# Kernel optimization log

Measured on AMD Instinct MI355X. Metric: run time of the kernel, lower is better.

The kernel has to match this reference:

```python
import jax, jax.numpy as jnp
import numpy as np

B = 2048            # reactions per batch
NODES_PER_MOL = 32
N = B * NODES_PER_MOL   # 65536 nodes per slot graph
E = 2 * N               # 131072 edges per slot graph
NODE_IN, EDGE_IN, H = 64, 16, 300
DEPTH = 3


def setup_inputs() -> dict:
    key = jax.random.key(0)
    ks = jax.random.split(key, 24)
    d = {}
    for i, s in enumerate(["r1", "r2", "p1"]):
        d[f"x_{s}"] = jax.random.normal(ks[4 * i], (N, NODE_IN), jnp.float32)
        d[f"e_{s}"] = jax.random.normal(ks[4 * i + 1], (E, EDGE_IN), jnp.float32)
        d[f"src_{s}"] = jax.random.randint(ks[4 * i + 2], (E,), 0, N, jnp.int32)
        d[f"dst_{s}"] = jax.random.randint(ks[4 * i + 3], (E,), 0, N, jnp.int32)
        d[f"seg_{s}"] = jnp.repeat(jnp.arange(B, dtype=jnp.int32), NODES_PER_MOL)
    s = 0.05
    d["Wn"] = jax.random.normal(ks[12], (NODE_IN, H), jnp.float32) * s
    d["bn"] = jnp.zeros((H,), jnp.float32)
    d["We"] = jax.random.normal(ks[13], (EDGE_IN, H), jnp.float32) * s
    d["be"] = jnp.zeros((H,), jnp.float32)
    d["W1"] = jax.random.normal(ks[14], (DEPTH, H, H), jnp.float32) * s
    d["b1"] = jnp.zeros((DEPTH, H), jnp.float32)
    d["W2"] = jax.random.normal(ks[15], (DEPTH, H, H), jnp.float32) * s
    d["b2"] = jnp.zeros((DEPTH, H), jnp.float32)
    return d


def _gin(x, e, src, dst, Wn, bn, We, be, W1, b1, W2, b2):
    # project_node_feats = Linear + ReLU ; project_edge_feats = Linear
    h = jax.nn.relu(x @ Wn + bn)           # [N, H]
    eh = e @ We + be                        # [E, H]
    n = x.shape[0]
    for l in range(DEPTH):
        # GINEConv (eps=0): agg = sum_{j->i} relu(h_j + e_ji); h = MLP(h + agg)
        m = jax.nn.relu(h[src] + eh)        # [E, H]
        agg = jax.ops.segment_sum(m, dst, num_segments=n)
        z = h + agg
        z = jax.nn.relu(z @ W1[l] + b1[l]) @ W2[l] + b2[l]
        if l < DEPTH - 1:
            z = jax.nn.relu(z)              # inter-layer ReLU (dropout = eval no-op)
        h = z
    return h


def reference(x_r1, e_r1, src_r1, dst_r1, seg_r1,
              x_r2, e_r2, src_r2, dst_r2, seg_r2,
              x_p1, e_p1, src_p1, dst_p1, seg_p1,
              Wn, bn, We, be, W1, b1, W2, b2):
    def pooled(x, e, src, dst, seg):
        h = _gin(x, e, src, dst, Wn, bn, We, be, W1, b1, W2, b2)
        # per-molecule sum pooling == the original ragged start:end slice + sum loop
        return jax.ops.segment_sum(h, seg, num_segments=B)   # [B, H]
    reactants = pooled(x_r1, e_r1, src_r1, dst_r1, seg_r1) + \
                pooled(x_r2, e_r2, src_r2, dst_r2, seg_r2)
    products = pooled(x_p1, e_p1, src_p1, dst_p1, seg_p1)
    reaction_feat = reactants - products
    return (reaction_feat, reactants, products)
```

## Files before the change

### kernel.cpp

```cpp
#include <hip/hip_runtime.h>

typedef _Float16 half8 __attribute__((ext_vector_type(8)));
typedef _Float16 half4 __attribute__((ext_vector_type(4)));
typedef float    f32x4 __attribute__((ext_vector_type(4)));

#define N_NODES 65536
#define N_EDGES 131072
#define BB      2048
#define HDIM    300
#define HPAD    320

__global__ __launch_bounds__(256) void prepack_w(const float* __restrict__ src,
                                                 _Float16* __restrict__ dst,
                                                 int Kpad, int Kreal) {
    int idx = blockIdx.x * 256 + threadIdx.x;
    int n = idx / Kpad, k = idx - n * Kpad;
    if (n >= 384) return;
    float v = (n < 300 && k < Kreal) ? src[k * 300 + n] : 0.f;
    dst[idx] = (_Float16)v;
}

__global__ __launch_bounds__(256) void cvt_x(const float* __restrict__ x,
                                             _Float16* __restrict__ xh, int n) {
    int i = blockIdx.x * 256 + threadIdx.x;
    if (i < n) xh[i] = (_Float16)x[i];
}

__global__ __launch_bounds__(256) void cvt_e_csr(const float* __restrict__ ein,
                                                 const int2* __restrict__ se,
                                                 _Float16* __restrict__ ecsr) {
    int i = blockIdx.x * 256 + threadIdx.x;
    if (i >= N_EDGES * 32) return;
    int k = i & 31, s = i >> 5;
    int e = se[s].y;
    ecsr[i] = (_Float16)(k < 16 ? ein[(size_t)e * 16 + k] : 0.f);
}

__device__ __forceinline__ void gload16(const _Float16* g, _Float16* l) {
    __builtin_amdgcn_global_load_lds(
        (const __attribute__((address_space(1))) void*)g,
        (__attribute__((address_space(3))) void*)l, 16, 0, 0);
}

template <bool RELU>
__global__ __launch_bounds__(256) void gemm_f16(
        const _Float16* __restrict__ A,
        const _Float16* __restrict__ Bp, const float* __restrict__ bias,
        _Float16* __restrict__ out, int M, int K) {
    __shared__ _Float16 lds[3][2][128 * 32];

    int bid = blockIdx.x;
    int xcd = bid & 7, grp = bid >> 3;
    int mt = xcd + 8 * (grp / 3);
    int nt = grp % 3;
    int m0 = mt * 128, n0 = nt * 128;
    int t = threadIdx.x;
    int lane = t & 63, w = t >> 6;
    int wr = w >> 1, wc = w & 1;

    int srow[2], sko[2];
    #pragma unroll
    for (int q = 0; q < 2; ++q) {
        int row = (w * 2 + q) * 16 + (lane >> 2);
        int ch = (lane & 3) ^ ((row >> 1) & 3);
        srow[q] = row; sko[q] = ch * 8;
    }

    f32x4 acc[4][4] = {};
    int NK = K >> 5;

    auto stage = [&](int buf, int k0) {
        #pragma unroll
        for (int q = 0; q < 2; ++q) {
            gload16(&A[(size_t)(m0 + srow[q]) * K + k0 + sko[q]], &lds[buf][0][(w * 2 + q) * 512]);
            gload16(&Bp[(size_t)(n0 + srow[q]) * K + k0 + sko[q]], &lds[buf][1][(w * 2 + q) * 512]);
        }
    };

    stage(0, 0);
    if (NK > 1) stage(1, 32);
    for (int kt = 0; kt < NK; ++kt) {
        int cur = kt % 3;
        if (kt + 2 < NK) {
            stage((kt + 2) % 3, (kt + 2) << 5);
            asm volatile("s_waitcnt vmcnt(8)" ::: "memory");
        } else if (kt + 1 < NK) {
            asm volatile("s_waitcnt vmcnt(4)" ::: "memory");
        } else {
            asm volatile("s_waitcnt vmcnt(0)" ::: "memory");
        }
        __builtin_amdgcn_s_barrier();
        __builtin_amdgcn_sched_barrier(0);

        int lr = lane & 15, hi = lane >> 4;
        half8 af[4], bf[4];
        #pragma unroll
        for (int i = 0; i < 4; ++i) {
            int row = wr * 64 + i * 16 + lr;
            int lk = (hi ^ ((row >> 1) & 3)) * 8;
            af[i] = *(const half8*)&lds[cur][0][row * 32 + lk];
        }
        #pragma unroll
        for (int j = 0; j < 4; ++j) {
            int row = wc * 64 + j * 16 + lr;
            int lk = (hi ^ ((row >> 1) & 3)) * 8;
            bf[j] = *(const half8*)&lds[cur][1][row * 32 + lk];
        }
        #pragma unroll
        for (int i = 0; i < 4; ++i)
            #pragma unroll
            for (int j = 0; j < 4; ++j)
                acc[i][j] = __builtin_amdgcn_mfma_f32_16x16x32_f16(af[i], bf[j], acc[i][j], 0, 0, 0);

        __builtin_amdgcn_sched_barrier(0);
        __builtin_amdgcn_s_barrier();
    }
    __builtin_amdgcn_sched_barrier(0);

    _Float16* ct = &lds[0][0][0];
    {
        int lr = lane & 15, lq = (lane >> 4) * 4;
        #pragma unroll
        for (int j = 0; j < 4; ++j) {
            int col = wc * 64 + j * 16 + lr;
            int gcol = n0 + col;
            float bv = (gcol < 300) ? bias[gcol] : 0.f;
            #pragma unroll
            for (int i = 0; i < 4; ++i) {
                int rbase = wr * 64 + i * 16 + lq;
                #pragma unroll
                for (int q = 0; q < 4; ++q) {
                    float v = acc[i][j][q] + bv;
                    if (RELU) v = v > 0.f ? v : 0.f;
                    if (gcol >= 300) v = 0.f;
                    ct[(rbase + q) * 128 + col] = (_Float16)v;
                }
            }
        }
    }
    __syncthreads();
    #pragma unroll
    for (int r = 0; r < 8; ++r) {
        int row = r * 16 + (t >> 4);
        int c8 = (t & 15) * 8;
        if (n0 + c8 < HPAD) {
            half8 v = *(const half8*)&ct[row * 128 + c8];
            *(half8*)&out[(size_t)(m0 + row) * HPAD + n0 + c8] = v;
        }
    }
}

__global__ __launch_bounds__(256) void hist_kernel(const int* __restrict__ dst,
                                                   int* __restrict__ counts) {
    int e = blockIdx.x * 256 + threadIdx.x;
    if (e < N_EDGES) atomicAdd(&counts[dst[e]], 1);
}

__global__ __launch_bounds__(256) void scan_block(const int* __restrict__ in,
                                                  int* __restrict__ partial,
                                                  int* __restrict__ bsum, int nb) {
    __shared__ int s[256];
    int b = blockIdx.x, t = threadIdx.x;
    int v = (b < nb) ? in[b * 256 + t] : 0;
    s[t] = v;
    __syncthreads();
    for (int o = 1; o < 256; o <<= 1) {
        int x = (t >= o) ? s[t - o] : 0;
        __syncthreads();
        s[t] += x;
        __syncthreads();
    }
    partial[b * 256 + t] = s[t] - v;
    if (t == 255 && bsum) bsum[b] = s[255];
}

__global__ __launch_bounds__(256) void add_offsets(const int* __restrict__ partial,
                                                   const int* __restrict__ boff,
                                                   int* __restrict__ rowptr) {
    int i = blockIdx.x * 256 + threadIdx.x;
    if (i < N_NODES) rowptr[i] = partial[i] + boff[i >> 8];
    if (i == 0) rowptr[N_NODES] = N_EDGES;
}

__global__ __launch_bounds__(256) void scatter_csr(const int* __restrict__ src,
                                                   const int* __restrict__ dst,
                                                   const int* __restrict__ rowptr,
                                                   int* __restrict__ cnt,
                                                   int2* __restrict__ se) {
    int e = blockIdx.x * 256 + threadIdx.x;
    if (e >= N_EDGES) return;
    int d = dst[e];
    int pos = atomicAdd(&cnt[d], 1);
    se[rowptr[d] + pos] = make_int2(src[e], e);
}

__global__ __launch_bounds__(320) void gather_z(
        const _Float16* __restrict__ h, const _Float16* __restrict__ ehcsr,
        const int2* __restrict__ se, const int* __restrict__ rowptr,
        _Float16* __restrict__ z, int nblocks) {
    int t = threadIdx.x;
    int c = t % 40, ns = t / 40;
    for (int node = blockIdx.x * 8 + ns; node < N_NODES; node += nblocks * 8) {
        int r0 = rowptr[node], r1 = rowptr[node + 1];
        half8 hn = *(const half8*)&h[(size_t)node * HPAD + c * 8];
        half8 acc = {};
        for (int s = r0; s < r1; s += 4) {
            int nb = r1 - s;
            int idx[4];
            idx[0] = s;
            idx[1] = s + (1 < nb ? 1 : 0);
            idx[2] = s + (2 < nb ? 2 : 0);
            idx[3] = s + (3 < nb ? 3 : 0);
            half8 hv[4], ev[4];
            #pragma unroll
            for (int u = 0; u < 4; ++u) {
                int sp = se[idx[u]].x;
                hv[u] = *(const half8*)&h[(size_t)sp * HPAD + c * 8];
                ev[u] = *(const half8*)&ehcsr[(size_t)idx[u] * HPAD + c * 8];
            }
            #pragma unroll
            for (int u = 0; u < 4; ++u) {
                half8 m = hv[u] + ev[u];
                #pragma unroll
                for (int j = 0; j < 8; ++j)
                    m[j] = m[j] > (_Float16)0 ? m[j] : (_Float16)0;
                if (u < nb) acc += m;
            }
        }
        half8 o = hn + acc;
        *(half8*)&z[(size_t)node * HPAD + c * 8] = o;
    }
}

__global__ __launch_bounds__(128) void pool_kernel(const _Float16* __restrict__ h,
                                                   float* __restrict__ out, int add) {
    int b = blockIdx.x, t = threadIdx.x;
    if (t >= 75) return;
    float a0 = 0, a1 = 0, a2 = 0, a3 = 0;
    for (int r = 0; r < 32; ++r) {
        half4 v = *(const half4*)&h[(size_t)(b * 32 + r) * HPAD + t * 4];
        a0 += (float)v[0]; a1 += (float)v[1]; a2 += (float)v[2]; a3 += (float)v[3];
    }
    f32x4 o = {a0, a1, a2, a3};
    if (add) o += *(f32x4*)&out[b * 300 + t * 4];
    *(f32x4*)&out[b * 300 + t * 4] = o;
}

__global__ __launch_bounds__(256) void diff_kernel(float* __restrict__ reaction,
                                                   const float* __restrict__ reactants,
                                                   const float* __restrict__ products, int n) {
    int i = blockIdx.x * 256 + threadIdx.x;
    if (i < n) reaction[i] = reactants[i] - products[i];
}

extern "C" void kernel_launch(void* const* d_in, const int* in_sizes, int n_in,
                              void* d_out, int out_size, void* d_ws, size_t ws_size,
                              hipStream_t stream) {
    const float* x[3]   = {(const float*)d_in[0], (const float*)d_in[5],  (const float*)d_in[10]};
    const float* ein[3] = {(const float*)d_in[1], (const float*)d_in[6],  (const float*)d_in[11]};
    const int*   src[3] = {(const int*)d_in[2],   (const int*)d_in[7],    (const int*)d_in[12]};
    const int*   dst[3] = {(const int*)d_in[3],   (const int*)d_in[8],    (const int*)d_in[13]};
    const float* Wn = (const float*)d_in[15];
    const float* bn = (const float*)d_in[16];
    const float* We = (const float*)d_in[17];
    const float* be = (const float*)d_in[18];
    const float* W1 = (const float*)d_in[19];
    const float* b1 = (const float*)d_in[20];
    const float* W2 = (const float*)d_in[21];
    const float* b2 = (const float*)d_in[22];

    char* ws = (char*)d_ws;
    size_t off = 0;
    auto alloc = [&](size_t bytes) {
        char* p = ws + off; off += (bytes + 1023) & ~(size_t)1023; return p;
    };
    _Float16* h     = (_Float16*)alloc((size_t)N_NODES * HPAD * 2);
    _Float16* zbuf  = (_Float16*)alloc((size_t)N_NODES * HPAD * 2);
    _Float16* tbuf  = (_Float16*)alloc((size_t)N_NODES * HPAD * 2);
    _Float16* ehcsr = (_Float16*)alloc((size_t)N_EDGES * HPAD * 2);
    int*      counts= (int*)alloc((size_t)N_NODES * 4);
    int*      part  = (int*)alloc((size_t)N_NODES * 4);
    int*      bsum  = (int*)alloc(256 * 4);
    int*      bpart = (int*)alloc(256 * 4);
    int*      bzero = (int*)alloc(4);
    int*      rowptr= (int*)alloc((size_t)(N_NODES + 1) * 4);
    int*      cnt   = (int*)alloc((size_t)N_NODES * 4);
    int2*     se    = (int2*)alloc((size_t)N_EDGES * 8);
    _Float16* Wt1   = (_Float16*)alloc((size_t)3 * 384 * HPAD * 2);
    _Float16* Wt2   = (_Float16*)alloc((size_t)3 * 384 * HPAD * 2);
    _Float16* Wnt   = (_Float16*)alloc((size_t)384 * 64 * 2);
    _Float16* Wet   = (_Float16*)alloc((size_t)384 * 32 * 2);
    _Float16* xh    = (_Float16*)zbuf;
    _Float16* ecsr  = (_Float16*)tbuf;

    if (off > ws_size) return;

    for (int l = 0; l < 3; ++l) {
        prepack_w<<<(384 * HPAD + 255) / 256, 256, 0, stream>>>(W1 + l * 90000, Wt1 + l * 384 * HPAD, HPAD, 300);
        prepack_w<<<(384 * HPAD + 255) / 256, 256, 0, stream>>>(W2 + l * 90000, Wt2 + l * 384 * HPAD, HPAD, 300);
    }
    prepack_w<<<(384 * 64 + 255) / 256, 256, 0, stream>>>(Wn, Wnt, 64, 64);
    prepack_w<<<(384 * 32 + 255) / 256, 256, 0, stream>>>(We, Wet, 32, 16);
    hipMemsetAsync(bzero, 0, 4, stream);

    float* outp      = (float*)d_out;
    float* reaction  = outp;
    float* reactants = outp + (size_t)BB * HDIM;
    float* products  = outp + (size_t)2 * BB * HDIM;

    const int EG = (N_EDGES + 255) / 256;
    for (int g = 0; g < 3; ++g) {
        cvt_x<<<(N_NODES * 64 + 255) / 256, 256, 0, stream>>>(x[g], xh, N_NODES * 64);
        gemm_f16<true><<<512 * 3, 256, 0, stream>>>(xh, Wnt, bn, h, N_NODES, 64);

        hipMemsetAsync(counts, 0, (size_t)N_NODES * 4, stream);
        hist_kernel<<<EG, 256, 0, stream>>>(dst[g], counts);
        scan_block<<<256, 256, 0, stream>>>(counts, part, bsum, 256);
        scan_block<<<1, 256, 0, stream>>>(bsum, bpart, bzero, 1);
        add_offsets<<<256, 256, 0, stream>>>(part, bpart, rowptr);
        hipMemsetAsync(cnt, 0, (size_t)N_NODES * 4, stream);
        scatter_csr<<<EG, 256, 0, stream>>>(src[g], dst[g], rowptr, cnt, se);

        cvt_e_csr<<<(N_EDGES * 32 + 255) / 256, 256, 0, stream>>>(ein[g], se, ecsr);
        gemm_f16<false><<<1024 * 3, 256, 0, stream>>>(ecsr, Wet, be, ehcsr, N_EDGES, 32);

        for (int l = 0; l < 3; ++l) {
            gather_z<<<2048, 320, 0, stream>>>(h, ehcsr, se, rowptr, zbuf, 2048);
            gemm_f16<true><<<512 * 3, 256, 0, stream>>>(zbuf, Wt1 + l * 384 * HPAD, b1 + l * 300, tbuf, N_NODES, HPAD);
            if (l < 2)
                gemm_f16<true ><<<512 * 3, 256, 0, stream>>>(tbuf, Wt2 + l * 384 * HPAD, b2 + l * 300, h, N_NODES, HPAD);
            else
                gemm_f16<false><<<512 * 3, 256, 0, stream>>>(tbuf, Wt2 + l * 384 * HPAD, b2 + l * 300, h, N_NODES, HPAD);
        }
        if (g == 0)      pool_kernel<<<BB, 128, 0, stream>>>(h, reactants, 0);
        else if (g == 1) pool_kernel<<<BB, 128, 0, stream>>>(h, reactants, 1);
        else             pool_kernel<<<BB, 128, 0, stream>>>(h, products, 0);
    }
    diff_kernel<<<((BB * HDIM) + 255) / 256, 256, 0, stream>>>(reaction, reactants, products, BB * HDIM);
}
```

Baseline: 1.116 ms.

## Sort nodes by in-degree bucket for balanced gather and restructure GEMM prefetch barrier

Builds the CSR by bucketing destination nodes by in-degree (capped at 15) and laying out their edge ranges contiguously per bucket. Gather warps then process nodes of similar degree together, which reduces divergence in the per-node edge loop. The change also drops the multi-kernel prefix scan for a bucket histogram plus a tiny serial scan. In the GEMM, the prefetch of stage kt+2 now issues after the barrier rather than before the wait, which removes the trailing per-iteration barrier. This keeps buffer-reuse safety with three LDS buffers but may shorten the overlap between loads and compute.

```diff
diff --git a/kernel.cpp b/kernel.cpp
--- a/kernel.cpp
+++ b/kernel.cpp
@@ -9,6 +9,12 @@
 #define BB      2048
 #define HDIM    300
 #define HPAD    320
+
+#define A_DHIST 0
+#define A_DBASE 16
+#define A_EBASE 32
+#define A_DCNT  48
+#define A_E15   64
 
 __global__ __launch_bounds__(256) void prepack_w(const float* __restrict__ src,
                                                  _Float16* __restrict__ dst,
@@ -81,16 +87,14 @@
     if (NK > 1) stage(1, 32);
     for (int kt = 0; kt < NK; ++kt) {
         int cur = kt % 3;
-        if (kt + 2 < NK) {
-            stage((kt + 2) % 3, (kt + 2) << 5);
-            asm volatile("s_waitcnt vmcnt(8)" ::: "memory");
-        } else if (kt + 1 < NK) {
+        if (kt + 1 < NK) {
             asm volatile("s_waitcnt vmcnt(4)" ::: "memory");
         } else {
             asm volatile("s_waitcnt vmcnt(0)" ::: "memory");
         }
         __builtin_amdgcn_s_barrier();
         __builtin_amdgcn_sched_barrier(0);
+        if (kt + 2 < NK) stage((kt + 2) % 3, (kt + 2) << 5);
 
         int lr = lane & 15, hi = lane >> 4;
         half8 af[4], bf[4];
@@ -111,11 +115,8 @@
             #pragma unroll
             for (int j = 0; j < 4; ++j)
                 acc[i][j] = __builtin_amdgcn_mfma_f32_16x16x32_f16(af[i], bf[j], acc[i][j], 0, 0, 0);
-
-        __builtin_amdgcn_sched_barrier(0);
-        __builtin_amdgcn_s_barrier();
-    }
-    __builtin_amdgcn_sched_barrier(0);
+    }
+    __syncthreads();
 
     _Float16* ct = &lds[0][0][0];
     {
@@ -156,52 +157,69 @@
     if (e < N_EDGES) atomicAdd(&counts[dst[e]], 1);
 }
 
-__global__ __launch_bounds__(256) void scan_block(const int* __restrict__ in,
-                                                  int* __restrict__ partial,
-                                                  int* __restrict__ bsum, int nb) {
-    __shared__ int s[256];
-    int b = blockIdx.x, t = threadIdx.x;
-    int v = (b < nb) ? in[b * 256 + t] : 0;
-    s[t] = v;
-    __syncthreads();
-    for (int o = 1; o < 256; o <<= 1) {
-        int x = (t >= o) ? s[t - o] : 0;
-        __syncthreads();
-        s[t] += x;
-        __syncthreads();
-    }
-    partial[b * 256 + t] = s[t] - v;
-    if (t == 255 && bsum) bsum[b] = s[255];
-}
-
-__global__ __launch_bounds__(256) void add_offsets(const int* __restrict__ partial,
-                                                   const int* __restrict__ boff,
-                                                   int* __restrict__ rowptr) {
-    int i = blockIdx.x * 256 + threadIdx.x;
-    if (i < N_NODES) rowptr[i] = partial[i] + boff[i >> 8];
-    if (i == 0) rowptr[N_NODES] = N_EDGES;
+__global__ __launch_bounds__(256) void bucket_hist(const int* __restrict__ counts,
+                                                   int* __restrict__ aux) {
+    int n = blockIdx.x * 256 + threadIdx.x;
+    if (n >= N_NODES) return;
+    int b = counts[n]; b = b < 15 ? b : 15;
+    atomicAdd(&aux[A_DHIST + b], 1);
+}
+
+__global__ void scan16(int* __restrict__ aux) {
+    if (threadIdx.x == 0) {
+        int acc = 0, eacc = 0;
+        for (int b = 0; b < 15; ++b) {
+            aux[A_DBASE + b] = acc;
+            aux[A_EBASE + b] = eacc;
+            acc  += aux[A_DHIST + b];
+            eacc += aux[A_DHIST + b] * b;
+        }
+        aux[A_DBASE + 15] = acc;
+        aux[A_EBASE + 15] = eacc;
+    }
+}
+
+__global__ __launch_bounds__(256) void place_nodes(const int* __restrict__ counts,
+                                                   int* __restrict__ aux,
+                                                   int* __restrict__ sortedid,
+                                                   int2* __restrict__ rptr,
+                                                   int* __restrict__ r0node) {
+    int n = blockIdx.x * 256 + threadIdx.x;
+    if (n >= N_NODES) return;
+    int deg = counts[n];
+    int b = deg < 15 ? deg : 15;
+    int pos = atomicAdd(&aux[A_DCNT + b], 1);
+    int i = aux[A_DBASE + b] + pos;
+    int r0;
+    if (b < 15) r0 = aux[A_EBASE + b] + pos * b;
+    else        r0 = aux[A_EBASE + 15] + atomicAdd(&aux[A_E15], deg);
+    sortedid[i] = n;
+    rptr[i] = make_int2(r0, deg);
+    r0node[n] = r0;
 }
 
 __global__ __launch_bounds__(256) void scatter_csr(const int* __restrict__ src,
                                                    const int* __restrict__ dst,
-                                                   const int* __restrict__ rowptr,
+                                                   const int* __restrict__ r0node,
                                                    int* __restrict__ cnt,
                                                    int2* __restrict__ se) {
     int e = blockIdx.x * 256 + threadIdx.x;
     if (e >= N_EDGES) return;
     int d = dst[e];
     int pos = atomicAdd(&cnt[d], 1);
-    se[rowptr[d] + pos] = make_int2(src[e], e);
+    se[r0node[d] + pos] = make_int2(src[e], e);
 }
 
 __global__ __launch_bounds__(320) void gather_z(
         const _Float16* __restrict__ h, const _Float16* __restrict__ ehcsr,
-        const int2* __restrict__ se, const int* __restrict__ rowptr,
-        _Float16* __restrict__ z, int nblocks) {
+        const int2* __restrict__ se, const int* __restrict__ sortedid,
+        const int2* __restrict__ rptr, _Float16* __restrict__ z, int nblocks) {
     int t = threadIdx.x;
     int c = t % 40, ns = t / 40;
-    for (int node = blockIdx.x * 8 + ns; node < N_NODES; node += nblocks * 8) {
-        int r0 = rowptr[node], r1 = rowptr[node + 1];
+    for (int i = blockIdx.x * 8 + ns; i < N_NODES; i += nblocks * 8) {
+        int node = sortedid[i];
+        int2 rr = rptr[i];
+        int r0 = rr.x, r1 = rr.x + rr.y;
         half8 hn = *(const half8*)&h[(size_t)node * HPAD + c * 8];
         half8 acc = {};
         for (int s = r0; s < r1; s += 4) {
@@ -279,12 +297,11 @@
     _Float16* tbuf  = (_Float16*)alloc((size_t)N_NODES * HPAD * 2);
     _Float16* ehcsr = (_Float16*)alloc((size_t)N_EDGES * HPAD * 2);
     int*      counts= (int*)alloc((size_t)N_NODES * 4);
-    int*      part  = (int*)alloc((size_t)N_NODES * 4);
-    int*      bsum  = (int*)alloc(256 * 4);
-    int*      bpart = (int*)alloc(256 * 4);
-    int*      bzero = (int*)alloc(4);
-    int*      rowptr= (int*)alloc((size_t)(N_NODES + 1) * 4);
     int*      cnt   = (int*)alloc((size_t)N_NODES * 4);
+    int*      aux   = (int*)alloc(256 * 4);
+    int*      sortedid = (int*)alloc((size_t)N_NODES * 4);
+    int2*     rptr  = (int2*)alloc((size_t)N_NODES * 8);
+    int*      r0node= (int*)alloc((size_t)N_NODES * 4);
     int2*     se    = (int2*)alloc((size_t)N_EDGES * 8);
     _Float16* Wt1   = (_Float16*)alloc((size_t)3 * 384 * HPAD * 2);
     _Float16* Wt2   = (_Float16*)alloc((size_t)3 * 384 * HPAD * 2);
@@ -301,7 +318,6 @@
     }
     prepack_w<<<(384 * 64 + 255) / 256, 256, 0, stream>>>(Wn, Wnt, 64, 64);
     prepack_w<<<(384 * 32 + 255) / 256, 256, 0, stream>>>(We, Wet, 32, 16);
-    hipMemsetAsync(bzero, 0, 4, stream);
 
     float* outp      = (float*)d_out;
     float* reaction  = outp;
@@ -309,23 +325,23 @@
     float* products  = outp + (size_t)2 * BB * HDIM;
 
     const int EG = (N_EDGES + 255) / 256;
+    const int NG = (N_NODES + 255) / 256;
     for (int g = 0; g < 3; ++g) {
         cvt_x<<<(N_NODES * 64 + 255) / 256, 256, 0, stream>>>(x[g], xh, N_NODES * 64);
         gemm_f16<true><<<512 * 3, 256, 0, stream>>>(xh, Wnt, bn, h, N_NODES, 64);
 
-        hipMemsetAsync(counts, 0, (size_t)N_NODES * 4, stream);
+        hipMemsetAsync(counts, 0, (size_t)(2 * N_NODES + 256) * 4, stream);
         hist_kernel<<<EG, 256, 0, stream>>>(dst[g], counts);
-        scan_block<<<256, 256, 0, stream>>>(counts, part, bsum, 256);
-        scan_block<<<1, 256, 0, stream>>>(bsum, bpart, bzero, 1);
-        add_offsets<<<256, 256, 0, stream>>>(part, bpart, rowptr);
-        hipMemsetAsync(cnt, 0, (size_t)N_NODES * 4, stream);
-        scatter_csr<<<EG, 256, 0, stream>>>(src[g], dst[g], rowptr, cnt, se);
+        bucket_hist<<<NG, 256, 0, stream>>>(counts, aux);
+        scan16<<<1, 64, 0, stream>>>(aux);
+        place_nodes<<<NG, 256, 0, stream>>>(counts, aux, sortedid, rptr, r0node);
+        scatter_csr<<<EG, 256, 0, stream>>>(src[g], dst[g], r0node, cnt, se);
 
         cvt_e_csr<<<(N_EDGES * 32 + 255) / 256, 256, 0, stream>>>(ein[g], se, ecsr);
         gemm_f16<false><<<1024 * 3, 256, 0, stream>>>(ecsr, Wet, be, ehcsr, N_EDGES, 32);
 
         for (int l = 0; l < 3; ++l) {
-            gather_z<<<2048, 320, 0, stream>>>(h, ehcsr, se, rowptr, zbuf, 2048);
+            gather_z<<<2048, 320, 0, stream>>>(h, ehcsr, se, sortedid, rptr, zbuf, 2048);
             gemm_f16<true><<<512 * 3, 256, 0, stream>>>(zbuf, Wt1 + l * 384 * HPAD, b1 + l * 300, tbuf, N_NODES, HPAD);
             if (l < 2)
                 gemm_f16<true ><<<512 * 3, 256, 0, stream>>>(tbuf, Wt2 + l * 384 * HPAD, b2 + l * 300, h, N_NODES, HPAD);
```

Result: slower. 3.092 ms (+177.2%).

## Fuse per-layer MLP GEMMs into one kernel keeping hidden tile in LDS

Applied to the files above, without the earlier changes.

Adds a fused_layer kernel that computes both MLP GEMMs for a 128-row tile, writing the ReLU intermediate into swizzled LDS instead of round-tripping through the tbuf global buffer. It also launches one kernel per layer instead of two. Fragments are loaded directly from global memory with no LDS staging or software pipelining, and each block carries 160 accumulators per thread, so it risks register pressure and weaker latency hiding. Separately, the gemm_f16 prefetch is moved after the barrier with a single trailing barrier. The two memsets are merged by placing cnt next to counts.

```diff
diff --git a/kernel.cpp b/kernel.cpp
--- a/kernel.cpp
+++ b/kernel.cpp
@@ -81,16 +81,14 @@
     if (NK > 1) stage(1, 32);
     for (int kt = 0; kt < NK; ++kt) {
         int cur = kt % 3;
-        if (kt + 2 < NK) {
-            stage((kt + 2) % 3, (kt + 2) << 5);
-            asm volatile("s_waitcnt vmcnt(8)" ::: "memory");
-        } else if (kt + 1 < NK) {
+        if (kt + 1 < NK) {
             asm volatile("s_waitcnt vmcnt(4)" ::: "memory");
         } else {
             asm volatile("s_waitcnt vmcnt(0)" ::: "memory");
         }
         __builtin_amdgcn_s_barrier();
         __builtin_amdgcn_sched_barrier(0);
+        if (kt + 2 < NK) stage((kt + 2) % 3, (kt + 2) << 5);
 
         int lr = lane & 15, hi = lane >> 4;
         half8 af[4], bf[4];
@@ -111,11 +109,8 @@
             #pragma unroll
             for (int j = 0; j < 4; ++j)
                 acc[i][j] = __builtin_amdgcn_mfma_f32_16x16x32_f16(af[i], bf[j], acc[i][j], 0, 0, 0);
-
-        __builtin_amdgcn_sched_barrier(0);
-        __builtin_amdgcn_s_barrier();
-    }
-    __builtin_amdgcn_sched_barrier(0);
+    }
+    __syncthreads();
 
     _Float16* ct = &lds[0][0][0];
     {
@@ -147,6 +142,106 @@
             half8 v = *(const half8*)&ct[row * 128 + c8];
             *(half8*)&out[(size_t)(m0 + row) * HPAD + n0 + c8] = v;
         }
+    }
+}
+
+__global__ __launch_bounds__(256, 2) void fused_layer(
+        const _Float16* __restrict__ z, const _Float16* __restrict__ W1p,
+        const float* __restrict__ b1, const _Float16* __restrict__ W2p,
+        const float* __restrict__ b2, _Float16* __restrict__ out, int lastrelu) {
+    __shared__ _Float16 tl[128 * 320];
+    int m0 = blockIdx.x * 128;
+    int t = threadIdx.x;
+    int lane = t & 63, w = t >> 6;
+    int wr = w >> 1, wcn = (w & 1) * 160;
+    int lr = lane & 15, hi = lane >> 4;
+
+    f32x4 acc[4][10];
+    #pragma unroll
+    for (int i = 0; i < 4; ++i)
+        #pragma unroll
+        for (int j = 0; j < 10; ++j) acc[i][j] = (f32x4){0.f, 0.f, 0.f, 0.f};
+
+    #pragma unroll 1
+    for (int kt = 0; kt < 10; ++kt) {
+        int kof = kt * 32 + hi * 8;
+        half8 af[4], bf[10];
+        #pragma unroll
+        for (int i = 0; i < 4; ++i)
+            af[i] = *(const half8*)&z[(size_t)(m0 + wr * 64 + i * 16 + lr) * HPAD + kof];
+        #pragma unroll
+        for (int j = 0; j < 10; ++j)
+            bf[j] = *(const half8*)&W1p[(size_t)(wcn + j * 16 + lr) * HPAD + kof];
+        #pragma unroll
+        for (int i = 0; i < 4; ++i)
+            #pragma unroll
+            for (int j = 0; j < 10; ++j)
+                acc[i][j] = __builtin_amdgcn_mfma_f32_16x16x32_f16(af[i], bf[j], acc[i][j], 0, 0, 0);
+    }
+    #pragma unroll
+    for (int j = 0; j < 10; ++j) {
+        int col = wcn + j * 16 + lr;
+        float bv = (col < 300) ? b1[col] : 0.f;
+        #pragma unroll
+        for (int i = 0; i < 4; ++i) {
+            int rbase = wr * 64 + i * 16 + hi * 4;
+            #pragma unroll
+            for (int q = 0; q < 4; ++q) {
+                float v = acc[i][j][q] + bv;
+                v = v > 0.f ? v : 0.f;
+                int row = rbase + q;
+                tl[row * 320 + ((((col >> 3) ^ (row & 7)) << 3) | (col & 7))] = (_Float16)v;
+            }
+        }
+    }
+    __syncthreads();
+
+    #pragma unroll
+    for (int i = 0; i < 4; ++i)
+        #pragma unroll
+        for (int j = 0; j < 10; ++j) acc[i][j] = (f32x4){0.f, 0.f, 0.f, 0.f};
+    #pragma unroll 1
+    for (int kt = 0; kt < 10; ++kt) {
+        int kof = kt * 32 + hi * 8;
+        half8 af[4], bf[10];
+        #pragma unroll
+        for (int i = 0; i < 4; ++i) {
+            int row = wr * 64 + i * 16 + lr;
+            af[i] = *(const half8*)&tl[row * 320 + ((((kof >> 3) ^ (row & 7)) << 3))];
+        }
+        #pragma unroll
+        for (int j = 0; j < 10; ++j)
+            bf[j] = *(const half8*)&W2p[(size_t)(wcn + j * 16 + lr) * HPAD + kof];
+        #pragma unroll
+        for (int i = 0; i < 4; ++i)
+            #pragma unroll
+            for (int j = 0; j < 10; ++j)
+                acc[i][j] = __builtin_amdgcn_mfma_f32_16x16x32_f16(af[i], bf[j], acc[i][j], 0, 0, 0);
+    }
+    __syncthreads();
+
+    #pragma unroll
+    for (int j = 0; j < 10; ++j) {
+        int col = wcn + j * 16 + lr;
+        float bv = (col < 300) ? b2[col] : 0.f;
+        #pragma unroll
+        for (int i = 0; i < 4; ++i) {
+            int rbase = wr * 64 + i * 16 + hi * 4;
+            #pragma unroll
+            for (int q = 0; q < 4; ++q) {
+                float v = acc[i][j][q] + bv;
+                if (lastrelu) v = v > 0.f ? v : 0.f;
+                if (col >= 300) v = 0.f;
+                int row = rbase + q;
+                tl[row * 320 + ((((col >> 3) ^ (row & 7)) << 3) | (col & 7))] = (_Float16)v;
+            }
+        }
+    }
+    __syncthreads();
+    for (int idx = t; idx < 128 * 40; idx += 256) {
+        int row = idx / 40, c = idx - row * 40;
+        half8 v = *(const half8*)&tl[row * 320 + ((c ^ (row & 7)) << 3)];
+        *(half8*)&out[(size_t)(m0 + row) * HPAD + c * 8] = v;
     }
 }
 
@@ -279,12 +374,12 @@
     _Float16* tbuf  = (_Float16*)alloc((size_t)N_NODES * HPAD * 2);
     _Float16* ehcsr = (_Float16*)alloc((size_t)N_EDGES * HPAD * 2);
     int*      counts= (int*)alloc((size_t)N_NODES * 4);
+    int*      cnt   = (int*)alloc((size_t)N_NODES * 4);
     int*      part  = (int*)alloc((size_t)N_NODES * 4);
     int*      bsum  = (int*)alloc(256 * 4);
     int*      bpart = (int*)alloc(256 * 4);
     int*      bzero = (int*)alloc(4);
     int*      rowptr= (int*)alloc((size_t)(N_NODES + 1) * 4);
-    int*      cnt   = (int*)alloc((size_t)N_NODES * 4);
     int2*     se    = (int2*)alloc((size_t)N_EDGES * 8);
     _Float16* Wt1   = (_Float16*)alloc((size_t)3 * 384 * HPAD * 2);
     _Float16* Wt2   = (_Float16*)alloc((size_t)3 * 384 * HPAD * 2);
@@ -313,12 +408,11 @@
         cvt_x<<<(N_NODES * 64 + 255) / 256, 256, 0, stream>>>(x[g], xh, N_NODES * 64);
         gemm_f16<true><<<512 * 3, 256, 0, stream>>>(xh, Wnt, bn, h, N_NODES, 64);
 
-        hipMemsetAsync(counts, 0, (size_t)N_NODES * 4, stream);
+        hipMemsetAsync(counts, 0, (size_t)2 * N_NODES * 4, stream);
         hist_kernel<<<EG, 256, 0, stream>>>(dst[g], counts);
         scan_block<<<256, 256, 0, stream>>>(counts, part, bsum, 256);
         scan_block<<<1, 256, 0, stream>>>(bsum, bpart, bzero, 1);
         add_offsets<<<256, 256, 0, stream>>>(part, bpart, rowptr);
-        hipMemsetAsync(cnt, 0, (size_t)N_NODES * 4, stream);
         scatter_csr<<<EG, 256, 0, stream>>>(src[g], dst[g], rowptr, cnt, se);
 
         cvt_e_csr<<<(N_EDGES * 32 + 255) / 256, 256, 0, stream>>>(ein[g], se, ecsr);
@@ -326,11 +420,8 @@
 
         for (int l = 0; l < 3; ++l) {
             gather_z<<<2048, 320, 0, stream>>>(h, ehcsr, se, rowptr, zbuf, 2048);
-            gemm_f16<true><<<512 * 3, 256, 0, stream>>>(zbuf, Wt1 + l * 384 * HPAD, b1 + l * 300, tbuf, N_NODES, HPAD);
-            if (l < 2)
-                gemm_f16<true ><<<512 * 3, 256, 0, stream>>>(tbuf, Wt2 + l * 384 * HPAD, b2 + l * 300, h, N_NODES, HPAD);
-            else
-                gemm_f16<false><<<512 * 3, 256, 0, stream>>>(tbuf, Wt2 + l * 384 * HPAD, b2 + l * 300, h, N_NODES, HPAD);
+            fused_layer<<<512, 256, 0, stream>>>(zbuf, Wt1 + l * 384 * HPAD, b1 + l * 300,
+                                                 Wt2 + l * 384 * HPAD, b2 + l * 300, h, l < 2);
         }
         if (g == 0)      pool_kernel<<<BB, 128, 0, stream>>>(h, reactants, 0);
         else if (g == 1) pool_kernel<<<BB, 128, 0, stream>>>(h, reactants, 1);
```

New measurement: 1.511 ms. 35.4% more time.
